# Optimization experiments

Measured on AMD Instinct MI355X. Metric: run time of the kernel, lower is better.

The kernel has to match this reference:

```python
import jax, jax.numpy as jnp
import numpy as np

H = 8            # head_size (hard-coded in the original forward)
BB = 0.6         # balance_bias
NEG = -1e9


def masked_softmax(x, m, axis=-1):
    # softmax over `axis`, zero out masked entries, renormalize
    p = jax.nn.softmax(x, axis=axis)
    p = p * m
    return p / (p.sum(axis=axis, keepdims=True) + 1e-13)


def setup_inputs():
    key = jax.random.key(0)
    ks = jax.random.split(key, 12)
    B, B0, V, A, Hd = 8, 2, 384, 384, 512
    S = V + A
    s = 1.0 / np.sqrt(Hd)
    return {
        'q': jax.random.normal(ks[0], (B, S, Hd), jnp.float32),
        'k': jax.random.normal(ks[1], (B, S, Hd), jnp.float32),
        'v': jax.random.normal(ks[2], (B, S, Hd), jnp.float32),
        'mask': jnp.ones((B, S, 1), jnp.float32),
        'depth_value': jax.random.uniform(ks[3], (B0, V), jnp.float32),
        'coord_3d': jax.random.normal(ks[4], (B, V, 3), jnp.float32),
        'va_v_mask': jnp.ones((B, V, 1), jnp.float32),
        'va_a_mask': jnp.ones((B, A, 1), jnp.float32),
        'mean_depth_value': jax.random.uniform(ks[5], (B, A), jnp.float32),
        'Wq': jax.random.normal(ks[6], (Hd, Hd), jnp.float32) * s,
        'bq': jnp.zeros((Hd,), jnp.float32),
        'Wk': jax.random.normal(ks[7], (Hd, Hd), jnp.float32) * s,
        'bk': jnp.zeros((Hd,), jnp.float32),
        'Wv': jax.random.normal(ks[8], (Hd, Hd), jnp.float32) * s,
        'bv': jnp.zeros((Hd,), jnp.float32),
        'Wo': jax.random.normal(ks[9], (Hd, Hd), jnp.float32) * s,
        'bo': jnp.zeros((Hd,), jnp.float32),
    }


def reference(q, k, v, mask, depth_value, coord_3d, va_v_mask, va_a_mask,
              mean_depth_value, Wq, bq, Wk, bk, Wv, bv, Wo, bo):
    B, S, Hd = q.shape
    d = Hd // H
    scale = d ** (-0.5)
    V = va_v_mask.shape[1]
    A = va_a_mask.shape[1]
    B0 = depth_value.shape[0]
    rep = B // B0  # = 4 in the original code

    qh = (q @ Wq + bq).reshape(B, S, H, d).transpose(0, 2, 1, 3)  # [B,H,S,d]
    kh = (k @ Wk + bk).reshape(B, S, H, d).transpose(0, 2, 1, 3)
    vh = (v @ Wv + bv).reshape(B, S, H, d).transpose(0, 2, 1, 3)

    m = mask[:, None]                      # [B,1,S,1]
    mask4 = m * jnp.swapaxes(m, 2, 3)      # [B,1,S,S] (broadcasts over heads)

    x = jnp.einsum('bhqd,bhkd->bhqk', qh, kh) * scale  # [B,H,S,S]

    # visual-visual depth bias
    dv = depth_value[:, :, None]                       # [B0,V,1]
    diff = jnp.abs(dv - jnp.swapaxes(dv, 1, 2))        # [B0,V,V]
    diff = jnp.repeat(diff, rep, axis=0)[:, None]      # [B,1,V,V]
    self_mask = 1.0 - jnp.eye(V, dtype=x.dtype)
    depth_term = jnp.abs(x[:, :, :V, :V]) * (jnp.exp(-diff) - BB) * self_mask  # [B,H,V,V]

    # audio->visual attention map (pre-bias scores)
    x_av = x[:, :, V:, :V]                             # [B,H,A,V]
    m_av = mask4[:, :, V:, :V]
    att_score_av = jnp.where(m_av > 0, x_av, NEG)
    att_map_av = masked_softmax(att_score_av, m_av, axis=3)

    # audio-visual depth bias (mean_depth_value branch)
    tdv = jnp.repeat(jnp.swapaxes(dv, 1, 2), rep, axis=0)           # [B,1,V]
    diff_va = jnp.abs(mean_depth_value[:, :, None] - tdv)[:, None]  # [B,1,A,V]
    depth_av_term = jnp.abs(x_av) * (jnp.exp(-diff_va) - BB)        # [B,H,A,V]

    # assemble bias matrix: [:V,:V]=depth_term, [V:,:V]=depth_av_term, rest 0
    top = jnp.concatenate([depth_term, jnp.zeros((B, H, V, S - V), x.dtype)], axis=3)
    bot = jnp.concatenate([depth_av_term, jnp.zeros((B, H, A, S - V), x.dtype)], axis=3)
    bias = jnp.concatenate([top, bot], axis=2)         # [B,H,S,S]

    x = x + bias
    att_score = jnp.where(mask4 > 0, x, NEG)
    att_map = masked_softmax(att_score, mask4 * jnp.ones((1, H, 1, 1), x.dtype), axis=3)
    out = jnp.einsum('bhqk,bhkd->bhqd', att_map, vh)   # [B,H,S,d]

    # auxiliary depth mean via the a->v attention map
    dv_rep = jnp.repeat(depth_value, rep, axis=0)      # [B,V]
    md = jnp.einsum('bhav,bv->bha', att_map_av, dv_rep)
    md = md.mean(axis=1)                               # [B,A]
    md = md.sum(axis=-1) / va_a_mask[:, :, 0].sum(axis=-1)  # [B]
    md = jnp.broadcast_to(md[:, None], (B, A))

    out = out.transpose(0, 2, 1, 3).reshape(B, S, H * d)
    out = out @ Wo + bo
    return out, att_score, att_map, md
```

## Files before the change

### kernel.cpp

```cpp
#include <hip/hip_runtime.h>
#include <hip/hip_bf16.h>
#include <cstdint>
#include <cstddef>

namespace {
constexpr int B  = 8;
constexpr int S  = 768;
constexpr int V  = 384;
constexpr int A  = 384;
constexpr int H  = 8;
constexpr int D  = 64;
constexpr int HD = 512;
constexpr float SCALE = 0.125f;
constexpr float BBC   = 0.6f;
constexpr float NEGV  = -1000000000.0f;
constexpr size_t N_QH = (size_t)B * H * S * D;
}

using short8 = __attribute__((ext_vector_type(8))) short;
using f32x4  = __attribute__((ext_vector_type(4))) float;

static __device__ __forceinline__ unsigned short f2bf(float f) {
  union { float f; unsigned int u; } v; v.f = f;
  unsigned int r = v.u + 0x7FFFu + ((v.u >> 16) & 1u);
  return (unsigned short)(r >> 16);
}
static __device__ __forceinline__ f32x4 mfma16(short8 a, short8 b, f32x4 c) {
  return __builtin_amdgcn_mfma_f32_16x16x32_bf16(a, b, c, 0, 0, 0);
}
static __device__ __forceinline__ short8 pack_bf8(float4 a, float4 b) {
  union { short8 s; uint4 u; } r;
  r.u.x = (unsigned)f2bf(a.x) | ((unsigned)f2bf(a.y) << 16);
  r.u.y = (unsigned)f2bf(a.z) | ((unsigned)f2bf(a.w) << 16);
  r.u.z = (unsigned)f2bf(b.x) | ((unsigned)f2bf(b.y) << 16);
  r.u.w = (unsigned)f2bf(b.z) | ((unsigned)f2bf(b.w) << 16);
  return r.s;
}
static __device__ __forceinline__ ushort4 pack_bf4(f32x4 a, float4 bi) {
  ushort4 r;
  r.x = f2bf(a[0] + bi.x); r.y = f2bf(a[1] + bi.y);
  r.z = f2bf(a[2] + bi.z); r.w = f2bf(a[3] + bi.w);
  return r;
}

__global__ __launch_bounds__(256) void prep_w(
    const float* __restrict__ Wq, const float* __restrict__ Wk,
    const float* __restrict__ Wv, const float* __restrict__ Wo,
    unsigned short* __restrict__ wt)
{
  __shared__ float tile[64][68];
  const int id = blockIdx.x;
  const int z = id >> 6, tl = id & 63;
  const int k0 = (tl >> 3) * 64, n0 = (tl & 7) * 64;
  const float* W = (z == 0) ? Wq : (z == 1) ? Wk : (z == 2) ? Wv : Wo;
  unsigned short* WT = wt + (size_t)z * 262144;
  const int t = threadIdx.x;
#pragma unroll
  for (int u = 0; u < 4; ++u) {
    int idx = u * 256 + t;
    int r = idx >> 4, c4 = (idx & 15) * 4;
    *(float4*)&tile[r][c4] = *(const float4*)&W[(size_t)(k0 + r) * 512 + n0 + c4];
  }
  __syncthreads();
#pragma unroll
  for (int u = 0; u < 4; ++u) {
    int idx = u * 256 + t;
    int n = idx >> 4, kq = (idx & 15) * 4;
    unsigned int h0 = f2bf(tile[kq + 0][n]), h1 = f2bf(tile[kq + 1][n]);
    unsigned int h2 = f2bf(tile[kq + 2][n]), h3 = f2bf(tile[kq + 3][n]);
    *(uint2*)&WT[(size_t)(n0 + n) * 512 + k0 + kq] =
        make_uint2(h0 | (h1 << 16), h2 | (h3 << 16));
  }
}

__global__ __launch_bounds__(256) void qkv_mfma(
    const float* __restrict__ q, const float* __restrict__ k,
    const float* __restrict__ v, const unsigned short* __restrict__ wt,
    const float* __restrict__ bq, const float* __restrict__ bk,
    const float* __restrict__ bv,
    unsigned short* __restrict__ qh, unsigned short* __restrict__ kh,
    unsigned short* __restrict__ vhT)
{
  __shared__ unsigned short Bh[64][40];
  __shared__ unsigned short Ax[64][40];
  const int lin = ((blockIdx.x & 7) * 288) + (blockIdx.x >> 3);
  const int n0 = (lin & 7) * 64;
  const int gidx = lin >> 3;
  const int mt = gidx % 96, z = gidx / 96;
  const int m0 = mt * 64;
  const float* X = (z == 0) ? q : (z == 1) ? k : v;
  const unsigned short* WT = wt + (size_t)z * 262144;
  const float* bias = (z == 0) ? bq : (z == 1) ? bk : bv;
  const int t = threadIdx.x, w = t >> 6, lane = t & 63;
  const int l15 = lane & 15, g = lane >> 4;
  const int bb = m0 / S;
  f32x4 acc[4] = {};

  const int srow = t >> 2, skq = (t & 3) * 8;
  for (int k0 = 0; k0 < 512; k0 += 32) {
    float4 x0 = *(const float4*)&X[(size_t)(m0 + srow) * 512 + k0 + skq];
    float4 x1 = *(const float4*)&X[(size_t)(m0 + srow) * 512 + k0 + skq + 4];
    short8 wrow = *(const short8*)&WT[(size_t)(n0 + srow) * 512 + k0 + skq];
    __syncthreads();
    *(short8*)&Ax[srow][skq] = pack_bf8(x0, x1);
    *(short8*)&Bh[srow][skq] = wrow;
    __syncthreads();
    if (z != 2) {
      short8 xfrag = *(short8*)&Ax[w * 16 + l15][g * 8];
#pragma unroll
      for (int tn = 0; tn < 4; ++tn) {
        short8 wfrag = *(short8*)&Bh[tn * 16 + l15][g * 8];
        acc[tn] = mfma16(wfrag, xfrag, acc[tn]);
      }
    } else {
      short8 wh = *(short8*)&Bh[w * 16 + l15][g * 8];
#pragma unroll
      for (int tm = 0; tm < 4; ++tm) {
        short8 xf = *(short8*)&Ax[tm * 16 + l15][g * 8];
        acc[tm] = mfma16(wh, xf, acc[tm]);
      }
    }
  }

  if (z != 2) {
    unsigned short* Y = (z == 0) ? qh : kh;
    const int s = m0 + w * 16 + l15 - bb * S;
    const int h = n0 >> 6;
    unsigned short* yrow = &Y[((size_t)(bb * H + h) * S + s) * D];
#pragma unroll
    for (int tn = 0; tn < 4; ++tn) {
      const int d0 = tn * 16 + g * 4;
      float4 bi4 = *(const float4*)&bias[n0 + d0];
      *(ushort4*)&yrow[d0] = pack_bf4(acc[tn], bi4);
    }
  } else {
#pragma unroll
    for (int tm = 0; tm < 4; ++tm) {
      const int mcol = m0 + tm * 16 + l15;
      const int s = mcol - bb * S;
#pragma unroll
      for (int r = 0; r < 4; ++r) {
        const int n = n0 + w * 16 + g * 4 + r;
        const int h = n >> 6, d = n & 63;
        vhT[((size_t)(bb * H + h) * D + d) * S + s] = f2bf(acc[tm][r] + bias[n]);
      }
    }
  }
}

__global__ __launch_bounds__(256, 4) void fused_attn(
    const unsigned short* __restrict__ qh, const unsigned short* __restrict__ kh,
    const unsigned short* __restrict__ vhT,
    const float* __restrict__ mask, const float* __restrict__ depth_value,
    const float* __restrict__ mean_depth,
    float* __restrict__ att_score, float* __restrict__ att_map,
    unsigned short* __restrict__ ctx, float* __restrict__ md_rows)
{
  __shared__ unsigned short Ps[16][768];
  __shared__ float mcol[768];
  __shared__ float dvcol[384];
  __shared__ float pmax[16][4];
  __shared__ float psum[16][4];
  __shared__ float psem[16][4];
  __shared__ float asmd[16][2];
  __shared__ float mxA[16], rdA[16], drefsA[16], mrwA[16];

  const int id = blockIdx.x;
  const int rest = id >> 3;
  const int rt = rest % 48;
  const int bh = (id & 7) + 8 * (rest / 48);
  const int b = bh >> 3, b0 = b >> 2;
  const int r0 = rt * 16;
  const int t = threadIdx.x;
  const int w = t >> 6;
  const int lane = t & 63;
  const int l15 = lane & 15, g = lane >> 4;
  const bool avblk = (r0 >= V);

  for (int j = t; j < 768; j += 256) mcol[j] = mask[(size_t)b * S + j];
  for (int j = t; j < 384; j += 256) dvcol[j] = depth_value[(size_t)b0 * V + j];
  if (t < 16) {
    const int row = r0 + t;
    drefsA[t] = (row < V) ? depth_value[(size_t)b0 * V + row]
                          : mean_depth[(size_t)b * A + (row - V)];
    mrwA[t] = mask[(size_t)b * S + row];
  }

  short8 qf[2];
#pragma unroll
  for (int ks = 0; ks < 2; ++ks)
    qf[ks] = *(const short8*)&qh[((size_t)bh * S + r0 + l15) * D + ks * 32 + g * 8];

  f32x4 acc[12] = {};
#pragma unroll
  for (int tn = 0; tn < 12; ++tn) {
    const int col = w * 192 + tn * 16 + l15;
#pragma unroll
    for (int ks = 0; ks < 2; ++ks) {
      short8 kf = *(const short8*)&kh[((size_t)bh * S + col) * D + ks * 32 + g * 8];
      acc[tn] = mfma16(qf[ks], kf, acc[tn]);
    }
  }
  __syncthreads();

  const bool biasw = (w < 2);
  float mcr[12], dvc[12];
#pragma unroll
  for (int tn = 0; tn < 12; ++tn) {
    const int col = w * 192 + tn * 16 + l15;
    mcr[tn] = mcol[col];
    dvc[tn] = biasw ? dvcol[col] : 0.f;
  }

#pragma unroll
  for (int r = 0; r < 4; ++r) {
    const int lrow = g * 4 + r;
    const int row = r0 + lrow;
    const float mr = mrwA[lrow];
    const float dref = drefsA[lrow];
    float* srow = &att_score[((size_t)bh * S + row) * S];
#pragma unroll
    for (int tn = 0; tn < 12; ++tn) {
      const int col = w * 192 + tn * 16 + l15;
      float x = acc[tn][r] * SCALE;
      if (biasw) {
        float gg = __expf(-fabsf(dref - dvc[tn])) - BBC;
        float bb2 = fabsf(x) * gg;
        if (row == col) bb2 = 0.f;
        x += bb2;
      }
      x = (mr * mcr[tn] > 0.f) ? x : NEGV;
      __builtin_nontemporal_store(x, &srow[col]);
      acc[tn][r] = x;
    }
  }

#pragma unroll
  for (int r = 0; r < 4; ++r) {
    float v = NEGV;
#pragma unroll
    for (int tn = 0; tn < 12; ++tn) v = fmaxf(v, acc[tn][r]);
#pragma unroll
    for (int o = 1; o < 16; o <<= 1) v = fmaxf(v, __shfl_xor(v, o, 16));
    if (l15 == 0) pmax[g * 4 + r][w] = v;
  }
  __syncthreads();
  if (t < 16)
    mxA[t] = fmaxf(fmaxf(pmax[t][0], pmax[t][1]), fmaxf(pmax[t][2], pmax[t][3]));
  __syncthreads();

  if (avblk) {
    if (biasw) {
#pragma unroll
      for (int r = 0; r < 4; ++r) {
        const int lrow = g * 4 + r;
        const float mdv = drefsA[lrow];
        const float mr = mrwA[lrow];
        const float amx = fmaxf(2.5f * mxA[lrow], 0.f);
        float se = 0.f, sem = 0.f, smd = 0.f;
#pragma unroll
        for (int tn = 0; tn < 12; ++tn) {
          float post = acc[tn][r];
          float gg = __expf(-fabsf(mdv - dvc[tn])) - BBC;
          float pre = post / (post > 0.f ? 1.f + gg : 1.f - gg);
          float pm = mr * mcr[tn];
          pre = (pm > 0.f) ? pre : NEGV;
          float e = __expf(pre - amx);
          se += e; sem += e * pm; smd += e * pm * dvc[tn];
        }
#pragma unroll
        for (int o = 1; o < 16; o <<= 1) {
          se += __shfl_xor(se, o, 16);
          sem += __shfl_xor(sem, o, 16);
          smd += __shfl_xor(smd, o, 16);
        }
        if (l15 == 0) { psum[lrow][w] = se; psem[lrow][w] = sem; asmd[lrow][w] = smd; }
      }
    }
    __syncthreads();
    if (t < 16) {
      float se = psum[t][0] + psum[t][1];
      float sem = psem[t][0] + psem[t][1];
      float smd = asmd[t][0] + asmd[t][1];
      md_rows[(size_t)bh * A + (r0 + t - V)] = smd / (sem + 1e-13f * se);
    }
    __syncthreads();
  }

#pragma unroll
  for (int r = 0; r < 4; ++r) {
    const int lrow = g * 4 + r;
    const float mx = mxA[lrow];
    const float mr = mrwA[lrow];
    float se = 0.f, sem = 0.f;
#pragma unroll
    for (int tn = 0; tn < 12; ++tn) {
      float e = __expf(acc[tn][r] - mx);
      acc[tn][r] = e;
      se += e; sem += e * (mr * mcr[tn]);
    }
#pragma unroll
    for (int o = 1; o < 16; o <<= 1) {
      se += __shfl_xor(se, o, 16);
      sem += __shfl_xor(sem, o, 16);
    }
    if (l15 == 0) { psum[lrow][w] = se; psem[lrow][w] = sem; }
  }
  __syncthreads();
  if (t < 16) {
    float se = psum[t][0] + psum[t][1] + psum[t][2] + psum[t][3];
    float sem = psem[t][0] + psem[t][1] + psem[t][2] + psem[t][3];
    rdA[t] = 1.f / (sem + 1e-13f * se);
  }
  __syncthreads();

#pragma unroll
  for (int r = 0; r < 4; ++r) {
    const int lrow = g * 4 + r;
    const int row = r0 + lrow;
    const float rden = rdA[lrow];
    const float mr = mrwA[lrow];
    float* prow = &att_map[((size_t)bh * S + row) * S];
    const int swz = (lrow & 7) << 4;
#pragma unroll
    for (int tn = 0; tn < 12; ++tn) {
      const int col = w * 192 + tn * 16 + l15;
      float p = acc[tn][r] * (mr * mcr[tn]) * rden;
      __builtin_nontemporal_store(p, &prow[col]);
      Ps[lrow][col ^ swz] = f2bf(p);
    }
  }
  __syncthreads();

  {
    const int aswz = (l15 & 7) << 4;
    f32x4 pacc = {};
    const unsigned short* vcol = &vhT[((size_t)bh * D + w * 16 + l15) * S];
#pragma unroll 8
    for (int kk = 0; kk < 24; ++kk) {
      short8 a = *(short8*)&Ps[l15][(kk * 32 + g * 8) ^ aswz];
      short8 bv = *(const short8*)&vcol[kk * 32 + g * 8];
      pacc = mfma16(a, bv, pacc);
    }
#pragma unroll
    for (int r = 0; r < 4; ++r) {
      const int row = r0 + g * 4 + r;
      ctx[((size_t)bh * S + row) * D + w * 16 + l15] = f2bf(pacc[r]);
    }
  }
}

__global__ __launch_bounds__(256) void gemm_out(
    const unsigned short* __restrict__ Xb, const unsigned short* __restrict__ WT,
    const float* __restrict__ bias, float* __restrict__ Yf,
    const float* __restrict__ md_rows, const float* __restrict__ va_a_mask,
    float* __restrict__ md_out)
{
  const int t = threadIdx.x;
  if (blockIdx.x >= 768) {
    __shared__ float red0[256];
    __shared__ float red1[256];
    const int b = blockIdx.x - 768;
    float s1 = 0.f, s2 = 0.f;
    for (int u = t; u < H * A; u += 256) s1 += md_rows[(size_t)b * H * A + u];
    for (int u = t; u < A; u += 256) s2 += va_a_mask[(size_t)b * A + u];
    red0[t] = s1; red1[t] = s2;
    __syncthreads();
    for (int o = 128; o > 0; o >>= 1) {
      if (t < o) { red0[t] += red0[t + o]; red1[t] += red1[t + o]; }
      __syncthreads();
    }
    const float val = red0[0] / ((float)H * red1[0]);
    for (int u = t; u < A; u += 256) md_out[(size_t)b * A + u] = val;
    return;
  }
  __shared__ unsigned short Bh[64][40];
  const int lin = ((blockIdx.x & 7) * 96) + (blockIdx.x >> 3);
  const int n0 = (lin & 7) * 64;
  const int m0 = (lin >> 3) * 64;
  const int w = t >> 6, lane = t & 63;
  const int l15 = lane & 15, g = lane >> 4;
  const int bb = m0 / S;
  f32x4 acc[4] = {};
  const int srow = t >> 2, skq = (t & 3) * 8;
  const int s = m0 + w * 16 + l15 - bb * S;
  for (int k0 = 0; k0 < 512; k0 += 32) {
    __syncthreads();
    *(short8*)&Bh[srow][skq] = *(const short8*)&WT[(size_t)(n0 + srow) * 512 + k0 + skq];
    __syncthreads();
    const int h = k0 >> 6, d = (k0 & 63) + g * 8;
    short8 ah = *(const short8*)&Xb[((size_t)(bb * H + h) * S + s) * D + d];
#pragma unroll
    for (int tn = 0; tn < 4; ++tn) {
      short8 bh_ = *(short8*)&Bh[tn * 16 + l15][g * 8];
      acc[tn] = mfma16(ah, bh_, acc[tn]);
    }
  }
#pragma unroll
  for (int tn = 0; tn < 4; ++tn) {
    const int c = n0 + tn * 16 + l15;
    const float bi = bias[c];
#pragma unroll
    for (int r = 0; r < 4; ++r) {
      const int m = m0 + w * 16 + g * 4 + r;
      Yf[(size_t)m * 512 + c] = acc[tn][r] + bi;
    }
  }
}

extern "C" void kernel_launch(void* const* d_in, const int* in_sizes, int n_in,
                              void* d_out, int out_size, void* d_ws, size_t ws_size,
                              hipStream_t stream) {
  const float* q           = (const float*)d_in[0];
  const float* k           = (const float*)d_in[1];
  const float* v           = (const float*)d_in[2];
  const float* mask        = (const float*)d_in[3];
  const float* depth_value = (const float*)d_in[4];
  const float* va_a_mask   = (const float*)d_in[7];
  const float* mean_depth  = (const float*)d_in[8];
  const float* Wq = (const float*)d_in[9];
  const float* bq = (const float*)d_in[10];
  const float* Wk = (const float*)d_in[11];
  const float* bk = (const float*)d_in[12];
  const float* Wv = (const float*)d_in[13];
  const float* bv = (const float*)d_in[14];
  const float* Wo = (const float*)d_in[15];
  const float* bo = (const float*)d_in[16];

  unsigned short* wsu = (unsigned short*)d_ws;
  unsigned short* qh  = wsu;
  unsigned short* kh  = wsu + N_QH;
  unsigned short* vhT = wsu + 2 * N_QH;
  unsigned short* ctx = qh;
  unsigned short* wt  = wsu + 3 * N_QH;
  float* md_rows = (float*)(wsu + 3 * N_QH + 4 * 262144);

  float* out       = (float*)d_out;
  float* att_score = out + (size_t)B * S * HD;
  float* att_map   = att_score + (size_t)B * H * S * S;
  float* md_out    = att_map + (size_t)B * H * S * S;

  prep_w<<<256, 256, 0, stream>>>(Wq, Wk, Wv, Wo, wt);
  qkv_mfma<<<2304, 256, 0, stream>>>(q, k, v, wt, bq, bk, bv, qh, kh, vhT);
  fused_attn<<<3072, 256, 0, stream>>>(qh, kh, vhT, mask, depth_value, mean_depth,
                                       att_score, att_map, ctx, md_rows);
  gemm_out<<<776, 256, 0, stream>>>(ctx, wt + 3 * 262144, bo, out,
                                    md_rows, va_a_mask, md_out);
}
```

Measured before the change: 155.4 us.

## Widen QKV GEMM tile to 128 columns and fold a->v depth-mean pass into score loop

```diff
diff --git a/kernel.cpp b/kernel.cpp
--- a/kernel.cpp
+++ b/kernel.cpp
@@ -81,11 +81,11 @@
     unsigned short* __restrict__ qh, unsigned short* __restrict__ kh,
     unsigned short* __restrict__ vhT)
 {
-  __shared__ unsigned short Bh[64][40];
+  __shared__ unsigned short Bh[128][40];
   __shared__ unsigned short Ax[64][40];
-  const int lin = ((blockIdx.x & 7) * 288) + (blockIdx.x >> 3);
-  const int n0 = (lin & 7) * 64;
-  const int gidx = lin >> 3;
+  const int lin = ((blockIdx.x & 7) * 144) + (blockIdx.x >> 3);
+  const int n0 = (lin & 3) * 128;
+  const int gidx = lin >> 2;
   const int mt = gidx % 96, z = gidx / 96;
   const int m0 = mt * 64;
   const float* X = (z == 0) ? q : (z == 1) ? k : v;
@@ -94,30 +94,34 @@
   const int t = threadIdx.x, w = t >> 6, lane = t & 63;
   const int l15 = lane & 15, g = lane >> 4;
   const int bb = m0 / S;
-  f32x4 acc[4] = {};
+  f32x4 acc[8] = {};
 
   const int srow = t >> 2, skq = (t & 3) * 8;
   for (int k0 = 0; k0 < 512; k0 += 32) {
     float4 x0 = *(const float4*)&X[(size_t)(m0 + srow) * 512 + k0 + skq];
     float4 x1 = *(const float4*)&X[(size_t)(m0 + srow) * 512 + k0 + skq + 4];
-    short8 wrow = *(const short8*)&WT[(size_t)(n0 + srow) * 512 + k0 + skq];
+    short8 wr0 = *(const short8*)&WT[(size_t)(n0 + srow) * 512 + k0 + skq];
+    short8 wr1 = *(const short8*)&WT[(size_t)(n0 + 64 + srow) * 512 + k0 + skq];
     __syncthreads();
     *(short8*)&Ax[srow][skq] = pack_bf8(x0, x1);
-    *(short8*)&Bh[srow][skq] = wrow;
+    *(short8*)&Bh[srow][skq] = wr0;
+    *(short8*)&Bh[64 + srow][skq] = wr1;
     __syncthreads();
     if (z != 2) {
       short8 xfrag = *(short8*)&Ax[w * 16 + l15][g * 8];
 #pragma unroll
-      for (int tn = 0; tn < 4; ++tn) {
+      for (int tn = 0; tn < 8; ++tn) {
         short8 wfrag = *(short8*)&Bh[tn * 16 + l15][g * 8];
         acc[tn] = mfma16(wfrag, xfrag, acc[tn]);
       }
     } else {
-      short8 wh = *(short8*)&Bh[w * 16 + l15][g * 8];
+      short8 wh0 = *(short8*)&Bh[(w * 2 + 0) * 16 + l15][g * 8];
+      short8 wh1 = *(short8*)&Bh[(w * 2 + 1) * 16 + l15][g * 8];
 #pragma unroll
       for (int tm = 0; tm < 4; ++tm) {
         short8 xf = *(short8*)&Ax[tm * 16 + l15][g * 8];
-        acc[tm] = mfma16(wh, xf, acc[tm]);
+        acc[tm]     = mfma16(wh0, xf, acc[tm]);
+        acc[4 + tm] = mfma16(wh1, xf, acc[4 + tm]);
       }
     }
   }
@@ -125,26 +129,27 @@
   if (z != 2) {
     unsigned short* Y = (z == 0) ? qh : kh;
     const int s = m0 + w * 16 + l15 - bb * S;
-    const int h = n0 >> 6;
-    unsigned short* yrow = &Y[((size_t)(bb * H + h) * S + s) * D];
-#pragma unroll
-    for (int tn = 0; tn < 4; ++tn) {
-      const int d0 = tn * 16 + g * 4;
-      float4 bi4 = *(const float4*)&bias[n0 + d0];
-      *(ushort4*)&yrow[d0] = pack_bf4(acc[tn], bi4);
+#pragma unroll
+    for (int tn = 0; tn < 8; ++tn) {
+      const int n = n0 + tn * 16 + g * 4;
+      const int h = n >> 6, d0 = n & 63;
+      float4 bi4 = *(const float4*)&bias[n];
+      *(ushort4*)&Y[((size_t)(bb * H + h) * S + s) * D + d0] = pack_bf4(acc[tn], bi4);
     }
   } else {
 #pragma unroll
-    for (int tm = 0; tm < 4; ++tm) {
-      const int mcol = m0 + tm * 16 + l15;
-      const int s = mcol - bb * S;
-#pragma unroll
-      for (int r = 0; r < 4; ++r) {
-        const int n = n0 + w * 16 + g * 4 + r;
-        const int h = n >> 6, d = n & 63;
-        vhT[((size_t)(bb * H + h) * D + d) * S + s] = f2bf(acc[tm][r] + bias[n]);
+    for (int j = 0; j < 2; ++j)
+#pragma unroll
+      for (int tm = 0; tm < 4; ++tm) {
+        const int mcol = m0 + tm * 16 + l15;
+        const int s = mcol - bb * S;
+#pragma unroll
+        for (int r = 0; r < 4; ++r) {
+          const int n = n0 + (w * 2 + j) * 16 + g * 4 + r;
+          const int h = n >> 6, d = n & 63;
+          vhT[((size_t)(bb * H + h) * D + d) * S + s] = f2bf(acc[j * 4 + tm][r] + bias[n]);
+        }
       }
-    }
   }
 }
 
@@ -219,11 +224,17 @@
     const float mr = mrwA[lrow];
     const float dref = drefsA[lrow];
     float* srow = &att_score[((size_t)bh * S + row) * S];
+    float se = 0.f, sem = 0.f, smd = 0.f;
 #pragma unroll
     for (int tn = 0; tn < 12; ++tn) {
       const int col = w * 192 + tn * 16 + l15;
       float x = acc[tn][r] * SCALE;
       if (biasw) {
+        if (avblk) {
+          float pm = mr * mcr[tn];
+          float e = (pm > 0.f) ? __expf(x) : 0.f;
+          se += e; sem += e * pm; smd += e * pm * dvc[tn];
+        }
         float gg = __expf(-fabsf(dref - dvc[tn])) - BBC;
         float bb2 = fabsf(x) * gg;
         if (row == col) bb2 = 0.f;
@@ -233,6 +244,15 @@
       __builtin_nontemporal_store(x, &srow[col]);
       acc[tn][r] = x;
     }
+    if (avblk && biasw) {
+#pragma unroll
+      for (int o = 1; o < 16; o <<= 1) {
+        se += __shfl_xor(se, o, 16);
+        sem += __shfl_xor(sem, o, 16);
+        smd += __shfl_xor(smd, o, 16);
+      }
+      if (l15 == 0) { psum[lrow][w] = se; psem[lrow][w] = sem; asmd[lrow][w] = smd; }
+    }
   }
 
 #pragma unroll
@@ -245,47 +265,16 @@
     if (l15 == 0) pmax[g * 4 + r][w] = v;
   }
   __syncthreads();
-  if (t < 16)
+  if (t < 16) {
     mxA[t] = fmaxf(fmaxf(pmax[t][0], pmax[t][1]), fmaxf(pmax[t][2], pmax[t][3]));
-  __syncthreads();
-
-  if (avblk) {
-    if (biasw) {
-#pragma unroll
-      for (int r = 0; r < 4; ++r) {
-        const int lrow = g * 4 + r;
-        const float mdv = drefsA[lrow];
-        const float mr = mrwA[lrow];
-        const float amx = fmaxf(2.5f * mxA[lrow], 0.f);
-        float se = 0.f, sem = 0.f, smd = 0.f;
-#pragma unroll
-        for (int tn = 0; tn < 12; ++tn) {
-          float post = acc[tn][r];
-          float gg = __expf(-fabsf(mdv - dvc[tn])) - BBC;
-          float pre = post / (post > 0.f ? 1.f + gg : 1.f - gg);
-          float pm = mr * mcr[tn];
-          pre = (pm > 0.f) ? pre : NEGV;
-          float e = __expf(pre - amx);
-          se += e; sem += e * pm; smd += e * pm * dvc[tn];
-        }
-#pragma unroll
-        for (int o = 1; o < 16; o <<= 1) {
-          se += __shfl_xor(se, o, 16);
-          sem += __shfl_xor(sem, o, 16);
-          smd += __shfl_xor(smd, o, 16);
-        }
-        if (l15 == 0) { psum[lrow][w] = se; psem[lrow][w] = sem; asmd[lrow][w] = smd; }
-      }
-    }
-    __syncthreads();
-    if (t < 16) {
+    if (avblk) {
       float se = psum[t][0] + psum[t][1];
       float sem = psem[t][0] + psem[t][1];
       float smd = asmd[t][0] + asmd[t][1];
       md_rows[(size_t)bh * A + (r0 + t - V)] = smd / (sem + 1e-13f * se);
     }
-    __syncthreads();
-  }
+  }
+  __syncthreads();
 
 #pragma unroll
   for (int r = 0; r < 4; ++r) {
@@ -441,7 +430,7 @@
   float* md_out    = att_map + (size_t)B * H * S * S;
 
   prep_w<<<256, 256, 0, stream>>>(Wq, Wk, Wv, Wo, wt);
-  qkv_mfma<<<2304, 256, 0, stream>>>(q, k, v, wt, bq, bk, bv, qh, kh, vhT);
+  qkv_mfma<<<1152, 256, 0, stream>>>(q, k, v, wt, bq, bk, bv, qh, kh, vhT);
   fused_attn<<<3072, 256, 0, stream>>>(qh, kh, vhT, mask, depth_value, mean_depth,
                                        att_score, att_map, ctx, md_rows);
   gemm_out<<<776, 256, 0, stream>>>(ctx, wt + 3 * 262144, bo, out,
```

Result: no change. 155.1 us (-0.2%).
